# Optimization experiments

Hardware: AMD Instinct MI355X
Metric: run time of the kernel (lower is better)

Reference implementation:

```python
import jax, jax.numpy as jnp
import numpy as np

B, S, D = 2, 512, 256

def setup_inputs() -> dict:
    key = jax.random.key(0)
    k1, k2, k3, k4, k5 = jax.random.split(key, 5)
    return {
        "query": jax.random.normal(k1, (B, S, D), dtype=jnp.float32),
        "key": jax.random.normal(k2, (B, S, D), dtype=jnp.float32),
        "value": jax.random.normal(k3, (B, S, D), dtype=jnp.float32),
        "Wm_w": jax.random.normal(k4, (D, D), dtype=jnp.float32) * (1.0 / np.sqrt(D)),
        "vm_w": jax.random.normal(k5, (1, D), dtype=jnp.float32) * (1.0 / np.sqrt(D)),
    }

def reference(query, key, value, Wm_w, vm_w):
    # pairwise difference: q.unsqueeze(1) - q.unsqueeze(2) -> [B, S, S, D]
    diff = query[:, None, :, :] - query[:, :, None, :]
    # Wm (Linear, no bias): [B,S,S,D] @ Wm_w^T, then tanh
    h = jnp.tanh(jnp.einsum('bijd,ed->bije', diff, Wm_w))
    # vm (Linear D->1, no bias) + squeeze -> scores [B, S, S]
    sjt = jnp.einsum('bije,e->bij', h, vm_w[0])
    # softmax over dim=2 (eval mode: dropout is identity)
    atten = jax.nn.softmax(sjt, axis=2)
    # bmm(atten, value) -> [B, S, D]
    context = jnp.einsum('bij,bjd->bid', atten, value)
    return context, atten
```

## Files before the change

### kernel.cpp

```cpp
#include <hip/hip_runtime.h>

#define B 2
#define S 512
#define D 256
#define C2L 2.885390081777927f
#define LOG2E 1.4426950408889634f

__global__ __launch_bounds__(256) void proj_kernel(const float* __restrict__ q,
                                                   const float* __restrict__ W,
                                                   float* __restrict__ PT,
                                                   float* __restrict__ P) {
    __shared__ float qlds[4 * D];
    const int t = threadIdx.x;
    const int b = blockIdx.x / (S / 4);
    const int i0 = (blockIdx.x % (S / 4)) * 4;
    const float* qbase = q + (size_t)(b * S + i0) * D;
    for (int idx = t; idx < 4 * D; idx += 256) qlds[idx] = qbase[idx];
    __syncthreads();
    const float* wr = W + (size_t)t * D;
    float a0 = 0.f, a1 = 0.f, a2 = 0.f, a3 = 0.f;
#pragma unroll 4
    for (int d = 0; d < D; ++d) {
        float w = wr[d];
        a0 = fmaf(qlds[d], w, a0);
        a1 = fmaf(qlds[D + d], w, a1);
        a2 = fmaf(qlds[2 * D + d], w, a2);
        a3 = fmaf(qlds[3 * D + d], w, a3);
    }
    a0 *= C2L; a1 *= C2L; a2 *= C2L; a3 *= C2L;
    float* p = PT + (size_t)(b * D + t) * S + i0;
    *(float4*)p = make_float4(a0, a1, a2, a3);
    if (P) {
        P[(size_t)(b * S + i0 + 0) * D + t] = a0;
        P[(size_t)(b * S + i0 + 1) * D + t] = a1;
        P[(size_t)(b * S + i0 + 2) * D + t] = a2;
        P[(size_t)(b * S + i0 + 3) * D + t] = a3;
    }
}

__global__ __launch_bounds__(512) void score_kernel(const float* __restrict__ PT,
                                                    const float* __restrict__ Psrc,
                                                    int rs, int es,
                                                    const float* __restrict__ vm,
                                                    float* __restrict__ sc) {
    __shared__ float vml[D], piA[D], piB[D];
    const int t = threadIdx.x;
    const int b = blockIdx.x >> 8;
    const int k = blockIdx.x & 255;
    const int rB = S - 1 - k;
    if (t < D) {
        vml[t] = vm[t];
        const size_t bo = (size_t)b * D * S;
        piA[t] = Psrc[bo + (size_t)k * rs + (size_t)t * es];
        piB[t] = Psrc[bo + (size_t)rB * rs + (size_t)t * es];
    }
    __syncthreads();

    const int segA = S - k;
    const bool inA = t < segA;
    const int row = inA ? k : rB;
    const int j = inA ? (k + t) : t;
    const float* pi = inA ? piA : piB;
    const float* pj = PT + (size_t)b * D * S + j;

    float acc = 0.f;
#pragma unroll 8
    for (int e = 0; e < D; ++e) {
        float d = pj[(size_t)e * S] - pi[e];
        float ex = __builtin_amdgcn_exp2f(d);
        float th = fmaf(-2.f, __builtin_amdgcn_rcpf(1.f + ex), 1.f);
        acc = fmaf(vml[e], th, acc);
    }
    float* sb = sc + (size_t)b * S * S;
    sb[(size_t)row * S + j] = acc;
    sb[(size_t)j * S + row] = -acc;
    if (t == 0) sb[(size_t)rB * S + rB] = 0.f;
}

__global__ __launch_bounds__(512) void softctx_kernel(float* __restrict__ att,
                                                      const float* __restrict__ value,
                                                      float* __restrict__ ctx) {
    __shared__ float a4[S][4];
    __shared__ float part[4][8][64][4];
    __shared__ float redm[4][2], reds[4][2];

    const int t = threadIdx.x;
    const int b = blockIdx.x >> 7;
    const int i0 = (blockIdx.x & 127) * 4;

    {
        const int row = t >> 7, jr = t & 127;
        const int lane = t & 63, half = (t >> 6) & 1;
        float* arow = att + (size_t)(b * S + i0 + row) * S;
        float s0 = arow[jr], s1 = arow[jr + 128], s2 = arow[jr + 256], s3 = arow[jr + 384];
        float lm = fmaxf(fmaxf(s0, s1), fmaxf(s2, s3));
#pragma unroll
        for (int off = 32; off; off >>= 1) lm = fmaxf(lm, __shfl_xor(lm, off));
        if (lane == 0) redm[row][half] = lm;
        __syncthreads();
        float m = fmaxf(redm[row][0], redm[row][1]);
        float p0 = __builtin_amdgcn_exp2f((s0 - m) * LOG2E);
        float p1 = __builtin_amdgcn_exp2f((s1 - m) * LOG2E);
        float p2 = __builtin_amdgcn_exp2f((s2 - m) * LOG2E);
        float p3 = __builtin_amdgcn_exp2f((s3 - m) * LOG2E);
        float ls = (p0 + p1) + (p2 + p3);
#pragma unroll
        for (int off = 32; off; off >>= 1) ls += __shfl_xor(ls, off);
        if (lane == 0) reds[row][half] = ls;
        __syncthreads();
        float rinv = __builtin_amdgcn_rcpf(reds[row][0] + reds[row][1]);
        p0 *= rinv; p1 *= rinv; p2 *= rinv; p3 *= rinv;
        arow[jr] = p0; arow[jr + 128] = p1; arow[jr + 256] = p2; arow[jr + 384] = p3;
        a4[jr][row] = p0; a4[jr + 128][row] = p1;
        a4[jr + 256][row] = p2; a4[jr + 384][row] = p3;
    }
    __syncthreads();

    {
        const int dq = t & 63, js = t >> 6;
        float4 acc0 = {}, acc1 = {}, acc2 = {}, acc3 = {};
        const float* vb = value + (size_t)b * S * D + (size_t)dq * 4;
#pragma unroll 4
        for (int jj = 0; jj < 64; ++jj) {
            int j = js * 64 + jj;
            float4 v = *(const float4*)(vb + (size_t)j * D);
            float w0 = a4[j][0], w1 = a4[j][1], w2 = a4[j][2], w3 = a4[j][3];
            acc0.x = fmaf(w0, v.x, acc0.x); acc0.y = fmaf(w0, v.y, acc0.y);
            acc0.z = fmaf(w0, v.z, acc0.z); acc0.w = fmaf(w0, v.w, acc0.w);
            acc1.x = fmaf(w1, v.x, acc1.x); acc1.y = fmaf(w1, v.y, acc1.y);
            acc1.z = fmaf(w1, v.z, acc1.z); acc1.w = fmaf(w1, v.w, acc1.w);
            acc2.x = fmaf(w2, v.x, acc2.x); acc2.y = fmaf(w2, v.y, acc2.y);
            acc2.z = fmaf(w2, v.z, acc2.z); acc2.w = fmaf(w2, v.w, acc2.w);
            acc3.x = fmaf(w3, v.x, acc3.x); acc3.y = fmaf(w3, v.y, acc3.y);
            acc3.z = fmaf(w3, v.z, acc3.z); acc3.w = fmaf(w3, v.w, acc3.w);
        }
        *(float4*)&part[0][js][dq][0] = acc0;
        *(float4*)&part[1][js][dq][0] = acc1;
        *(float4*)&part[2][js][dq][0] = acc2;
        *(float4*)&part[3][js][dq][0] = acc3;
    }
    __syncthreads();
    if (t < 256) {
        const int row = t >> 6, dq = t & 63;
        float4 sum = {};
#pragma unroll
        for (int js = 0; js < 8; ++js) {
            float4 p = *(const float4*)&part[row][js][dq][0];
            sum.x += p.x; sum.y += p.y; sum.z += p.z; sum.w += p.w;
        }
        *(float4*)(ctx + (size_t)(b * S + i0 + row) * D + (size_t)dq * 4) = sum;
    }
}

extern "C" void kernel_launch(void* const* d_in, const int* in_sizes, int n_in,
                              void* d_out, int out_size, void* d_ws, size_t ws_size,
                              hipStream_t stream) {
    const float* q = (const float*)d_in[0];
    const float* value = (const float*)d_in[2];
    const float* W = (const float*)d_in[3];
    const float* vm = (const float*)d_in[4];

    float* ctx = (float*)d_out;
    float* att = ctx + (size_t)B * S * D;
    float* PT = (float*)d_ws;
    const size_t ptsz = (size_t)B * D * S;
    bool haveP = ws_size >= 2u * ptsz * sizeof(float);
    float* P = haveP ? PT + ptsz : nullptr;

    proj_kernel<<<B * (S / 4), 256, 0, stream>>>(q, W, PT, P);
    if (haveP)
        score_kernel<<<B * (S / 2), 512, 0, stream>>>(PT, P, D, 1, vm, att);
    else
        score_kernel<<<B * (S / 2), 512, 0, stream>>>(PT, PT, 1, S, vm, att);
    softctx_kernel<<<B * (S / 4), 512, 0, stream>>>(att, value, ctx);
}
```

Baseline: 47.76 us.

## Factor tanh exponent into precomputed exp terms and pair rows per score block

The projection kernel now stores exp2 of the projected query (EJ) next to the raw projection. The score kernel then forms tanh through the product exp(pj)*exp(-pi), so the per-element exp goes away and only reciprocals remain. One reciprocal uses the hardware rcp and the other a Newton-iterated bit-trick estimate, which spreads work off the transcendental unit. Each 1024-thread block now handles two row pairs and splits the e-dimension between two halves reduced through LDS, and antisymmetry gives the transposed entries via -2*sum(vm) minus d. This risks overflow or precision loss when exp of large projected values is multiplied, and the workspace-size fallback is removed.

```diff
diff --git a/kernel.cpp b/kernel.cpp
--- a/kernel.cpp
+++ b/kernel.cpp
@@ -8,7 +8,7 @@
 
 __global__ __launch_bounds__(256) void proj_kernel(const float* __restrict__ q,
                                                    const float* __restrict__ W,
-                                                   float* __restrict__ PT,
+                                                   float* __restrict__ EJ,
                                                    float* __restrict__ P) {
     __shared__ float qlds[4 * D];
     const int t = threadIdx.x;
@@ -28,53 +28,95 @@
         a3 = fmaf(qlds[3 * D + d], w, a3);
     }
     a0 *= C2L; a1 *= C2L; a2 *= C2L; a3 *= C2L;
-    float* p = PT + (size_t)(b * D + t) * S + i0;
-    *(float4*)p = make_float4(a0, a1, a2, a3);
-    if (P) {
-        P[(size_t)(b * S + i0 + 0) * D + t] = a0;
-        P[(size_t)(b * S + i0 + 1) * D + t] = a1;
-        P[(size_t)(b * S + i0 + 2) * D + t] = a2;
-        P[(size_t)(b * S + i0 + 3) * D + t] = a3;
-    }
-}
-
-__global__ __launch_bounds__(512) void score_kernel(const float* __restrict__ PT,
-                                                    const float* __restrict__ Psrc,
-                                                    int rs, int es,
-                                                    const float* __restrict__ vm,
-                                                    float* __restrict__ sc) {
-    __shared__ float vml[D], piA[D], piB[D];
+    float* ej = EJ + (size_t)(b * D + t) * S + i0;
+    *(float4*)ej = make_float4(__builtin_amdgcn_exp2f(a0), __builtin_amdgcn_exp2f(a1),
+                               __builtin_amdgcn_exp2f(a2), __builtin_amdgcn_exp2f(a3));
+    P[(size_t)(b * S + i0 + 0) * D + t] = a0;
+    P[(size_t)(b * S + i0 + 1) * D + t] = a1;
+    P[(size_t)(b * S + i0 + 2) * D + t] = a2;
+    P[(size_t)(b * S + i0 + 3) * D + t] = a3;
+}
+
+__global__ __launch_bounds__(1024) void score_kernel(const float* __restrict__ EJ,
+                                                     const float* __restrict__ P,
+                                                     const float* __restrict__ vm,
+                                                     float* __restrict__ sc) {
+    __shared__ float4 fA[D], fB[D];
+    __shared__ float2 comb[2][S];
+    __shared__ float cred[16];
+
     const int t = threadIdx.x;
-    const int b = blockIdx.x >> 8;
-    const int k = blockIdx.x & 255;
-    const int rB = S - 1 - k;
+    const int b = blockIdx.x >> 7;
+    const int m = blockIdx.x & 127;
+    const int r0 = 2 * m, r1 = r0 + 1;
+    const int q0 = 510 - 2 * m, q1 = q0 + 1;
+    const int segA = 511 - 2 * m;
+
+    float pc = 0.f;
     if (t < D) {
-        vml[t] = vm[t];
-        const size_t bo = (size_t)b * D * S;
-        piA[t] = Psrc[bo + (size_t)k * rs + (size_t)t * es];
-        piB[t] = Psrc[bo + (size_t)rB * rs + (size_t)t * es];
-    }
-    __syncthreads();
-
-    const int segA = S - k;
-    const bool inA = t < segA;
-    const int row = inA ? k : rB;
-    const int j = inA ? (k + t) : t;
-    const float* pi = inA ? piA : piB;
-    const float* pj = PT + (size_t)b * D * S + j;
-
-    float acc = 0.f;
+        const size_t bP = (size_t)b * S * D;
+        float v = vm[t];
+        pc = v;
+        fA[t] = make_float4(__builtin_amdgcn_exp2f(-P[bP + (size_t)r0 * D + t]),
+                            __builtin_amdgcn_exp2f(-P[bP + (size_t)r1 * D + t]),
+                            -2.f * v, 0.f);
+        fB[t] = make_float4(__builtin_amdgcn_exp2f(-P[bP + (size_t)q0 * D + t]),
+                            __builtin_amdgcn_exp2f(-P[bP + (size_t)q1 * D + t]),
+                            -2.f * v, 0.f);
+    }
+#pragma unroll
+    for (int off = 32; off; off >>= 1) pc += __shfl_xor(pc, off);
+    if ((t & 63) == 0) cred[t >> 6] = pc;
+    __syncthreads();
+    float c = 0.f;
+#pragma unroll
+    for (int wv = 0; wv < 16; ++wv) c += cred[wv];
+
+    const int eh = t >> 9;
+    const int s = t & 511;
+    const bool inA = s < segA;
+    const int j = inA ? (r0 + 1 + s) : s;
+    const float4* ff = inA ? fA : fB;
+    const float* ej = EJ + (size_t)b * D * S + j;
+
+    float a0 = 0.f, a1 = 0.f;
+    const int e0 = eh * 128;
 #pragma unroll 8
-    for (int e = 0; e < D; ++e) {
-        float d = pj[(size_t)e * S] - pi[e];
-        float ex = __builtin_amdgcn_exp2f(d);
-        float th = fmaf(-2.f, __builtin_amdgcn_rcpf(1.f + ex), 1.f);
-        acc = fmaf(vml[e], th, acc);
-    }
+    for (int e = e0; e < e0 + 128; ++e) {
+        float ev = ej[(size_t)e * S];
+        float4 f = ff[e];
+        float x0 = ev * f.x;
+        float x1 = ev * f.y;
+        float y0 = 1.f + x0;
+        float y1 = 1.f + x1;
+        float rv = __builtin_amdgcn_rcpf(y0);
+        float rn = __uint_as_float(0x7EF311C3u - __float_as_uint(y1));
+        rn = rn * fmaf(-y1, rn, 2.f);
+        rn = rn * fmaf(-y1, rn, 2.f);
+        a0 = fmaf(f.z, rv, a0);
+        a1 = fmaf(f.z, rn, a1);
+    }
+    comb[eh][s] = make_float2(a0, a1);
+    __syncthreads();
+
     float* sb = sc + (size_t)b * S * S;
-    sb[(size_t)row * S + j] = acc;
-    sb[(size_t)j * S + row] = -acc;
-    if (t == 0) sb[(size_t)rB * S + rB] = 0.f;
+    {
+        float2 vL = comb[0][s], vH = comb[1][s];
+        float d0 = vL.x + vH.x, d1 = vL.y + vH.y;
+        const int rr0 = inA ? r0 : q0;
+        const int rr1 = inA ? r1 : q1;
+        if (eh == 0) {
+            sb[(size_t)rr0 * S + j] = d0;
+            sb[(size_t)rr1 * S + j] = d1;
+        } else {
+            *(float2*)&sb[(size_t)j * S + rr0] =
+                make_float2(fmaf(-2.f, c, -d0), fmaf(-2.f, c, -d1));
+        }
+    }
+    if (t < 2) {
+        const int rr = (t == 0) ? r0 : q0;
+        sb[(size_t)rr * S + rr] = -c;
+    }
 }
 
 __global__ __launch_bounds__(512) void softctx_kernel(float* __restrict__ att,
@@ -162,15 +204,10 @@
 
     float* ctx = (float*)d_out;
     float* att = ctx + (size_t)B * S * D;
-    float* PT = (float*)d_ws;
-    const size_t ptsz = (size_t)B * D * S;
-    bool haveP = ws_size >= 2u * ptsz * sizeof(float);
-    float* P = haveP ? PT + ptsz : nullptr;
-
-    proj_kernel<<<B * (S / 4), 256, 0, stream>>>(q, W, PT, P);
-    if (haveP)
-        score_kernel<<<B * (S / 2), 512, 0, stream>>>(PT, P, D, 1, vm, att);
-    else
-        score_kernel<<<B * (S / 2), 512, 0, stream>>>(PT, PT, 1, S, vm, att);
+    float* EJ = (float*)d_ws;
+    float* P = EJ + (size_t)B * D * S;
+
+    proj_kernel<<<B * (S / 4), 256, 0, stream>>>(q, W, EJ, P);
+    score_kernel<<<B * 128, 1024, 0, stream>>>(EJ, P, vm, att);
     softctx_kernel<<<B * (S / 4), 512, 0, stream>>>(att, value, ctx);
 }
```

After: 41.74 us. 1.14x faster.

## Factor tanh via precomputed exponentials and tile scores with 8-row register blocking

Applied to the files above, without the earlier changes.

Precomputes exp(2p) and exp(-2p) per projected element in the projection kernel, so each pairwise tanh becomes a single FMA plus reciprocal instead of exp, add and rcp. The score kernel now splits the embedding dimension into four parts that write separate partial score planes. It stages E tiles in LDS and register-blocks 8 query rows per thread, exploiting antisymmetry with a constant correction. The diagonal 8x8 blocks are computed directly in the projection kernel, and the softmax kernel sums the four partial planes. This trades more workspace traffic, a four-plane reduction, and an exp(+-x) overflow risk for far fewer transcendental ops and fewer strided global loads.

```diff
diff --git a/kernel.cpp b/kernel.cpp
--- a/kernel.cpp
+++ b/kernel.cpp
@@ -5,80 +5,170 @@
 #define D 256
 #define C2L 2.885390081777927f
 #define LOG2E 1.4426950408889634f
-
-__global__ __launch_bounds__(256) void proj_kernel(const float* __restrict__ q,
-                                                   const float* __restrict__ W,
-                                                   float* __restrict__ PT,
-                                                   float* __restrict__ P) {
-    __shared__ float qlds[4 * D];
+#define NEQ 4
+#define EQL (D / NEQ)
+#define ETILE 32
+
+__global__ __launch_bounds__(512, 2) void proj_kernel(const float* __restrict__ q,
+                                                      const float* __restrict__ W,
+                                                      const float* __restrict__ vm,
+                                                      float* __restrict__ EJ,
+                                                      float* __restrict__ EN,
+                                                      float* __restrict__ SC0) {
+    __shared__ float qlds[8][D];
+    __shared__ float ptl[8][D + 4];
+    __shared__ float vml[D];
+    __shared__ float dred[64][9];
+
     const int t = threadIdx.x;
-    const int b = blockIdx.x / (S / 4);
-    const int i0 = (blockIdx.x % (S / 4)) * 4;
-    const float* qbase = q + (size_t)(b * S + i0) * D;
-    for (int idx = t; idx < 4 * D; idx += 256) qlds[idx] = qbase[idx];
-    __syncthreads();
-    const float* wr = W + (size_t)t * D;
+    const int b = blockIdx.x >> 6;
+    const int g = blockIdx.x & 63;
+    const int i0 = g * 8;
+
+    {
+        const int row = t >> 6, c4 = (t & 63) * 4;
+        *(float4*)&qlds[row][c4] =
+            *(const float4*)(q + ((size_t)(b * S + i0 + row)) * D + c4);
+    }
+    if (t < D) vml[t] = -2.f * vm[t];
+    __syncthreads();
+
+    const int e = t & 255, rh = (t >> 8) * 4;
+    const float* wr = W + (size_t)e * D;
     float a0 = 0.f, a1 = 0.f, a2 = 0.f, a3 = 0.f;
 #pragma unroll 4
-    for (int d = 0; d < D; ++d) {
-        float w = wr[d];
-        a0 = fmaf(qlds[d], w, a0);
-        a1 = fmaf(qlds[D + d], w, a1);
-        a2 = fmaf(qlds[2 * D + d], w, a2);
-        a3 = fmaf(qlds[3 * D + d], w, a3);
+    for (int d = 0; d < D; d += 4) {
+        float4 w4 = *(const float4*)(wr + d);
+        float4 qa = *(const float4*)&qlds[rh + 0][d];
+        float4 qb = *(const float4*)&qlds[rh + 1][d];
+        float4 qc = *(const float4*)&qlds[rh + 2][d];
+        float4 qd = *(const float4*)&qlds[rh + 3][d];
+        a0 = fmaf(qa.x, w4.x, fmaf(qa.y, w4.y, fmaf(qa.z, w4.z, fmaf(qa.w, w4.w, a0))));
+        a1 = fmaf(qb.x, w4.x, fmaf(qb.y, w4.y, fmaf(qb.z, w4.z, fmaf(qb.w, w4.w, a1))));
+        a2 = fmaf(qc.x, w4.x, fmaf(qc.y, w4.y, fmaf(qc.z, w4.z, fmaf(qc.w, w4.w, a2))));
+        a3 = fmaf(qd.x, w4.x, fmaf(qd.y, w4.y, fmaf(qd.z, w4.z, fmaf(qd.w, w4.w, a3))));
     }
     a0 *= C2L; a1 *= C2L; a2 *= C2L; a3 *= C2L;
-    float* p = PT + (size_t)(b * D + t) * S + i0;
-    *(float4*)p = make_float4(a0, a1, a2, a3);
-    if (P) {
-        P[(size_t)(b * S + i0 + 0) * D + t] = a0;
-        P[(size_t)(b * S + i0 + 1) * D + t] = a1;
-        P[(size_t)(b * S + i0 + 2) * D + t] = a2;
-        P[(size_t)(b * S + i0 + 3) * D + t] = a3;
-    }
-}
-
-__global__ __launch_bounds__(512) void score_kernel(const float* __restrict__ PT,
-                                                    const float* __restrict__ Psrc,
-                                                    int rs, int es,
-                                                    const float* __restrict__ vm,
-                                                    float* __restrict__ sc) {
-    __shared__ float vml[D], piA[D], piB[D];
+    *(float4*)(EJ + ((size_t)(b * D + e)) * S + i0 + rh) =
+        make_float4(__builtin_amdgcn_exp2f(a0), __builtin_amdgcn_exp2f(a1),
+                    __builtin_amdgcn_exp2f(a2), __builtin_amdgcn_exp2f(a3));
+    EN[((size_t)(b * S + i0 + rh + 0)) * D + e] = __builtin_amdgcn_exp2f(-a0);
+    EN[((size_t)(b * S + i0 + rh + 1)) * D + e] = __builtin_amdgcn_exp2f(-a1);
+    EN[((size_t)(b * S + i0 + rh + 2)) * D + e] = __builtin_amdgcn_exp2f(-a2);
+    EN[((size_t)(b * S + i0 + rh + 3)) * D + e] = __builtin_amdgcn_exp2f(-a3);
+    ptl[rh + 0][e] = a0; ptl[rh + 1][e] = a1;
+    ptl[rh + 2][e] = a2; ptl[rh + 3][e] = a3;
+    __syncthreads();
+
+    {
+        const int ent = t & 63, r = ent >> 3, jj = ent & 7, ck = t >> 6;
+        float acc = 0.f;
+#pragma unroll 8
+        for (int el = ck * 32; el < ck * 32 + 32; ++el) {
+            float x = ptl[jj][el] - ptl[r][el];
+            float y = 1.f + __builtin_amdgcn_exp2f(x);
+            acc = fmaf(vml[el], __builtin_amdgcn_rcpf(y), acc);
+        }
+        dred[ent][ck] = acc;
+    }
+    __syncthreads();
+    if (t < 64) {
+        float sum = 0.f;
+#pragma unroll
+        for (int k = 0; k < 8; ++k) sum += dred[t][k];
+        SC0[(size_t)b * S * S + (size_t)(i0 + (t >> 3)) * S + i0 + (t & 7)] = sum;
+    }
+}
+
+__global__ __launch_bounds__(512, 2) void score_kernel(const float* __restrict__ EJ,
+                                                       const float* __restrict__ EN,
+                                                       const float* __restrict__ vm,
+                                                       float* __restrict__ SC) {
+    __shared__ float buf[ETILE][S];
+    __shared__ float ft[2][ETILE][8];
+    __shared__ float wlt[ETILE];
+    __shared__ float ceqL;
+
     const int t = threadIdx.x;
-    const int b = blockIdx.x >> 8;
-    const int k = blockIdx.x & 255;
-    const int rB = S - 1 - k;
-    if (t < D) {
-        vml[t] = vm[t];
-        const size_t bo = (size_t)b * D * S;
-        piA[t] = Psrc[bo + (size_t)k * rs + (size_t)t * es];
-        piB[t] = Psrc[bo + (size_t)rB * rs + (size_t)t * es];
-    }
-    __syncthreads();
-
-    const int segA = S - k;
-    const bool inA = t < segA;
-    const int row = inA ? k : rB;
-    const int j = inA ? (k + t) : t;
-    const float* pi = inA ? piA : piB;
-    const float* pj = PT + (size_t)b * D * S + j;
-
-    float acc = 0.f;
+    const int bid = blockIdx.x;
+    const int b = bid >> 7;
+    const int eq = (bid >> 5) & 3;
+    const int m = bid & 31;
+    const int e0 = eq * EQL;
+
+    const int NA = 504 - 8 * m;
+    const int NB = (m == 31) ? 0 : 8 + 8 * m;
+    const int rbA = 8 * m, rbB = 496 - 8 * m;
+
+    if (t < 64) {
+        float v = vm[e0 + t];
+#pragma unroll
+        for (int off = 32; off; off >>= 1) v += __shfl_xor(v, off);
+        if (t == 0) ceqL = v;
+    }
+
+    const bool act = t < NA + NB;
+    const bool inA = t < NA;
+    const int j = inA ? (8 * m + 8 + t) : t;
+    const int g = inA ? 0 : 1;
+
+    float acc[8] = {};
+#pragma unroll
+    for (int tile = 0; tile < EQL / ETILE; ++tile) {
+        const int et = e0 + tile * ETILE;
+        {
+            const int c4 = (t & 127) * 4, er = t >> 7;
+#pragma unroll
+            for (int p = 0; p < 8; ++p) {
+                const int el = p * 4 + er;
+                *(float4*)&buf[el][c4] =
+                    *(const float4*)(EJ + ((size_t)(b * D + et + el)) * S + c4);
+            }
+        }
+        {
+            const int gg = t >> 8, el = (t >> 3) & 31, r = t & 7;
+            const int rb = gg ? rbB : rbA;
+            ft[gg][el][r] = EN[((size_t)(b * S + rb + r)) * D + et + el];
+            if (t < ETILE) wlt[t] = -2.f * vm[et + t];
+        }
+        __syncthreads();
+        if (act) {
 #pragma unroll 8
-    for (int e = 0; e < D; ++e) {
-        float d = pj[(size_t)e * S] - pi[e];
-        float ex = __builtin_amdgcn_exp2f(d);
-        float th = fmaf(-2.f, __builtin_amdgcn_rcpf(1.f + ex), 1.f);
-        acc = fmaf(vml[e], th, acc);
-    }
-    float* sb = sc + (size_t)b * S * S;
-    sb[(size_t)row * S + j] = acc;
-    sb[(size_t)j * S + row] = -acc;
-    if (t == 0) sb[(size_t)rB * S + rB] = 0.f;
-}
-
-__global__ __launch_bounds__(512) void softctx_kernel(float* __restrict__ att,
+            for (int el = 0; el < ETILE; ++el) {
+                float ev = buf[el][j];
+                float w = wlt[el];
+                float4 fa = *(const float4*)&ft[g][el][0];
+                float4 fb = *(const float4*)&ft[g][el][4];
+                acc[0] = fmaf(w, __builtin_amdgcn_rcpf(fmaf(ev, fa.x, 1.f)), acc[0]);
+                acc[1] = fmaf(w, __builtin_amdgcn_rcpf(fmaf(ev, fa.y, 1.f)), acc[1]);
+                acc[2] = fmaf(w, __builtin_amdgcn_rcpf(fmaf(ev, fa.z, 1.f)), acc[2]);
+                acc[3] = fmaf(w, __builtin_amdgcn_rcpf(fmaf(ev, fa.w, 1.f)), acc[3]);
+                acc[4] = fmaf(w, __builtin_amdgcn_rcpf(fmaf(ev, fb.x, 1.f)), acc[4]);
+                acc[5] = fmaf(w, __builtin_amdgcn_rcpf(fmaf(ev, fb.y, 1.f)), acc[5]);
+                acc[6] = fmaf(w, __builtin_amdgcn_rcpf(fmaf(ev, fb.z, 1.f)), acc[6]);
+                acc[7] = fmaf(w, __builtin_amdgcn_rcpf(fmaf(ev, fb.w, 1.f)), acc[7]);
+            }
+        }
+        __syncthreads();
+    }
+    if (act) {
+        const float ceq = ceqL;
+        const int rb = inA ? rbA : rbB;
+        float* sb = SC + ((size_t)eq * B + b) * S * S;
+#pragma unroll
+        for (int k = 0; k < 8; ++k) sb[(size_t)(rb + k) * S + j] = acc[k];
+        *(float4*)&sb[(size_t)j * S + rb] =
+            make_float4(fmaf(-2.f, ceq, -acc[0]), fmaf(-2.f, ceq, -acc[1]),
+                        fmaf(-2.f, ceq, -acc[2]), fmaf(-2.f, ceq, -acc[3]));
+        *(float4*)&sb[(size_t)j * S + rb + 4] =
+            make_float4(fmaf(-2.f, ceq, -acc[4]), fmaf(-2.f, ceq, -acc[5]),
+                        fmaf(-2.f, ceq, -acc[6]), fmaf(-2.f, ceq, -acc[7]));
+    }
+}
+
+__global__ __launch_bounds__(512) void softctx_kernel(const float* __restrict__ SC,
                                                       const float* __restrict__ value,
+                                                      float* __restrict__ att,
                                                       float* __restrict__ ctx) {
     __shared__ float a4[S][4];
     __shared__ float part[4][8][64][4];
@@ -87,22 +177,31 @@
     const int t = threadIdx.x;
     const int b = blockIdx.x >> 7;
     const int i0 = (blockIdx.x & 127) * 4;
+    const size_t BSS = (size_t)B * S * S;
 
     {
         const int row = t >> 7, jr = t & 127;
         const int lane = t & 63, half = (t >> 6) & 1;
-        float* arow = att + (size_t)(b * S + i0 + row) * S;
-        float s0 = arow[jr], s1 = arow[jr + 128], s2 = arow[jr + 256], s3 = arow[jr + 384];
-        float lm = fmaxf(fmaxf(s0, s1), fmaxf(s2, s3));
+        const int i = i0 + row, gi = i >> 3;
+        const float* s0 = SC + (size_t)(b * S + i) * S;
+        float v[4];
+#pragma unroll
+        for (int o = 0; o < 4; ++o) {
+            const int j = jr + o * 128;
+            float v0 = s0[j];
+            float vs = v0 + s0[j + BSS] + s0[j + 2 * BSS] + s0[j + 3 * BSS];
+            v[o] = ((j >> 3) == gi) ? v0 : vs;
+        }
+        float lm = fmaxf(fmaxf(v[0], v[1]), fmaxf(v[2], v[3]));
 #pragma unroll
         for (int off = 32; off; off >>= 1) lm = fmaxf(lm, __shfl_xor(lm, off));
         if (lane == 0) redm[row][half] = lm;
         __syncthreads();
-        float m = fmaxf(redm[row][0], redm[row][1]);
-        float p0 = __builtin_amdgcn_exp2f((s0 - m) * LOG2E);
-        float p1 = __builtin_amdgcn_exp2f((s1 - m) * LOG2E);
-        float p2 = __builtin_amdgcn_exp2f((s2 - m) * LOG2E);
-        float p3 = __builtin_amdgcn_exp2f((s3 - m) * LOG2E);
+        float mx = fmaxf(redm[row][0], redm[row][1]);
+        float p0 = __builtin_amdgcn_exp2f((v[0] - mx) * LOG2E);
+        float p1 = __builtin_amdgcn_exp2f((v[1] - mx) * LOG2E);
+        float p2 = __builtin_amdgcn_exp2f((v[2] - mx) * LOG2E);
+        float p3 = __builtin_amdgcn_exp2f((v[3] - mx) * LOG2E);
         float ls = (p0 + p1) + (p2 + p3);
 #pragma unroll
         for (int off = 32; off; off >>= 1) ls += __shfl_xor(ls, off);
@@ -110,6 +209,7 @@
         __syncthreads();
         float rinv = __builtin_amdgcn_rcpf(reds[row][0] + reds[row][1]);
         p0 *= rinv; p1 *= rinv; p2 *= rinv; p3 *= rinv;
+        float* arow = att + (size_t)(b * S + i) * S;
         arow[jr] = p0; arow[jr + 128] = p1; arow[jr + 256] = p2; arow[jr + 384] = p3;
         a4[jr][row] = p0; a4[jr + 128][row] = p1;
         a4[jr + 256][row] = p2; a4[jr + 384][row] = p3;
@@ -162,15 +262,11 @@
 
     float* ctx = (float*)d_out;
     float* att = ctx + (size_t)B * S * D;
-    float* PT = (float*)d_ws;
-    const size_t ptsz = (size_t)B * D * S;
-    bool haveP = ws_size >= 2u * ptsz * sizeof(float);
-    float* P = haveP ? PT + ptsz : nullptr;
-
-    proj_kernel<<<B * (S / 4), 256, 0, stream>>>(q, W, PT, P);
-    if (haveP)
-        score_kernel<<<B * (S / 2), 512, 0, stream>>>(PT, P, D, 1, vm, att);
-    else
-        score_kernel<<<B * (S / 2), 512, 0, stream>>>(PT, PT, 1, S, vm, att);
-    softctx_kernel<<<B * (S / 4), 512, 0, stream>>>(att, value, ctx);
-}
+    float* EJ = (float*)d_ws;
+    float* EN = EJ + (size_t)B * D * S;
+    float* SC = EN + (size_t)B * S * D;
+
+    proj_kernel<<<B * 64, 512, 0, stream>>>(q, W, vm, EJ, EN, SC);
+    score_kernel<<<B * 128, 512, 0, stream>>>(EJ, EN, vm, SC);
+    softctx_kernel<<<B * 128, 512, 0, stream>>>(SC, value, att, ctx);
+}
```

Result: slower. 49.14 us (+2.9%).
